# Kernel tuning notes

Measured on AMD Instinct MI355X. Metric: run time of the kernel, lower is better.

## Reference

```python
import jax, jax.numpy as jnp
import numpy as np

N = 8192
IN_DIM = 512
HID = 256


def _gcn_conv(x, adj, W, b, drop):
    # x: [N, d_in] -> [N, d_out]
    h = jnp.matmul(x, W) + b
    if drop:
        return h
    # adj_hat = adj + I; deg = rowsum(adj_hat); out = D^-1/2 adj_hat D^-1/2 h
    deg = jnp.sum(adj, axis=1) + 1.0  # +1 from identity
    dinv = jnp.where(deg > 0, deg ** -0.5, 0.0)  # [N]
    hs = dinv[:, None] * h
    agg = jnp.matmul(adj, hs) + hs  # (adj + I) @ hs without materializing adj+I
    return dinv[:, None] * agg


def _layernorm(x, gamma, beta, eps=1e-6):
    mu = jnp.mean(x, axis=-1, keepdims=True)
    var = jnp.mean((x - mu) ** 2, axis=-1, keepdims=True)
    return (x - mu) * jax.lax.rsqrt(var + eps) * gamma + beta


def setup_inputs() -> dict:
    key = jax.random.key(0)
    ks = jax.random.split(key, 6)
    x = jax.random.normal(ks[0], (N, IN_DIM), dtype=jnp.float32)
    adj = jax.random.uniform(ks[1], (N, N), dtype=jnp.float32)
    W1 = jax.random.normal(ks[2], (IN_DIM, HID), dtype=jnp.float32) * (1.0 / np.sqrt(IN_DIM))
    b1 = jax.random.normal(ks[3], (HID,), dtype=jnp.float32) * 1e-6
    W2 = jax.random.normal(ks[4], (HID, HID), dtype=jnp.float32) * (1.0 / np.sqrt(HID))
    b2 = jax.random.normal(ks[5], (HID,), dtype=jnp.float32) * 1e-6
    ln_gamma = jnp.ones((HID,), dtype=jnp.float32)
    ln_beta = jnp.zeros((HID,), dtype=jnp.float32)
    return {"x": x, "adj": adj, "W1": W1, "b1": b1, "W2": W2, "b2": b2,
            "ln_gamma": ln_gamma, "ln_beta": ln_beta, "drop": 0}


def reference(x, adj, W1, b1, W2, b2, ln_gamma, ln_beta, drop):
    h = _gcn_conv(x, adj, W1, b1, drop)
    h = jax.nn.gelu(h, approximate=False)  # torch F.gelu default = exact erf
    h = _layernorm(h, ln_gamma, ln_beta)
    # dropout -> identity (eval / deterministic baseline)
    out = _gcn_conv(h, adj, W2, b2, drop)
    return out
```

## Files before the change

kernel.cpp:

```cpp
#include <hip/hip_runtime.h>
#include <math.h>

typedef __attribute__((ext_vector_type(4))) float f32x4;
typedef __attribute__((ext_vector_type(8))) short s16x8;
typedef __attribute__((ext_vector_type(2))) int i32x2;
typedef __attribute__((ext_vector_type(4))) int i32x4;

#define BM 32
#define BN 256
#define BK 64
#define LDS_TILE ((BM + BN) * BK)

#define BM2 128
#define BN2 256
#define BK2 128
#define KFULL 8192
#define ZSPLIT 4
#define KQ (KFULL / ZSPLIT)
#define ABYTES (BM2 * BK2)
#define BBYTES (BN2 * BK2)
#define BUFB (ABYTES + BBYTES)

#define SHS 2048.0f
#define INVQ (1.0f / (127.0f * 2048.0f))
#define INVSHS (1.0f / 2048.0f)

__device__ __forceinline__ unsigned short f2bf(float f) {
  unsigned int u = __float_as_uint(f);
  u += 0x7fffu + ((u >> 16) & 1u);
  return (unsigned short)(u >> 16);
}
__device__ __forceinline__ float bf2f(unsigned short h) {
  unsigned int u = ((unsigned int)h) << 16;
  return __uint_as_float(u);
}
__device__ __forceinline__ int rne_i(float x) {
  return __float_as_int(x + 12582912.0f) - 0x4B400000;
}
__device__ __forceinline__ int q_hs(float v) {
  int q = rne_i(v * SHS);
  return q < -127 ? -127 : (q > 127 ? 127 : q);
}
__device__ __forceinline__ void gload16(const void* g, void* l) {
  __builtin_amdgcn_global_load_lds(
      (const __attribute__((address_space(1))) void*)g,
      (__attribute__((address_space(3))) void*)l, 16, 0, 0);
}

__global__ __launch_bounds__(256) void transW(const float* __restrict__ W1,
                                              const float* __restrict__ W2,
                                              float* __restrict__ W1T,
                                              float* __restrict__ W2T) {
  __shared__ float t[64][65];
  int bx = blockIdx.x;
  const float* in;
  float* out;
  int K, M;
  if (bx < 32) { in = W1; out = W1T; K = 512; M = 256; }
  else { bx -= 32; in = W2; out = W2T; K = 256; M = 256; }
  int tiles_m = M >> 6;
  int tk = bx / tiles_m, tm = bx % tiles_m;
  int k0 = tk * 64, m0 = tm * 64;
  int ty = threadIdx.x >> 4, tx = threadIdx.x & 15;
#pragma unroll
  for (int i = 0; i < 4; ++i) {
    f32x4 v = *(const f32x4*)(in + (size_t)(k0 + ty + 16 * i) * M + m0 + tx * 4);
    t[ty + 16 * i][tx * 4 + 0] = v[0];
    t[ty + 16 * i][tx * 4 + 1] = v[1];
    t[ty + 16 * i][tx * 4 + 2] = v[2];
    t[ty + 16 * i][tx * 4 + 3] = v[3];
  }
  __syncthreads();
#pragma unroll
  for (int i = 0; i < 4; ++i) {
    int m = ty + 16 * i;
    f32x4 v = {t[tx * 4 + 0][m], t[tx * 4 + 1][m], t[tx * 4 + 2][m], t[tx * 4 + 3][m]};
    *(f32x4*)(out + (size_t)(m0 + m) * K + k0 + tx * 4) = v;
  }
}

template <bool BF32, int EPI>
__device__ __forceinline__ void gemm_small(int bx, unsigned short* ldsb,
                                           const float* __restrict__ AT,
                                           const void* __restrict__ BTp,
                                           void* __restrict__ outp,
                                           const float* __restrict__ bias,
                                           const float* __restrict__ dinv,
                                           int M, int N, int K) {
  const int tid = threadIdx.x;
  const int m0 = (bx & (M / BM - 1)) * BM;
  const int n0 = (bx / (M / BM)) * BN;
  const int sr = tid >> 3;
  const int sc = (tid & 7) * 8;
  const float* Bf = (const float*)BTp;
  const unsigned short* Bh = (const unsigned short*)BTp;

  f32x4 a_f[2];
  f32x4 b_f[8][2];
  s16x8 b_h[8];

  auto stage_load = [&](int k0) {
    const float* pa = AT + (size_t)(m0 + sr) * K + k0 + sc;
    a_f[0] = *(const f32x4*)(pa);
    a_f[1] = *(const f32x4*)(pa + 4);
#pragma unroll
    for (int it = 0; it < 8; ++it) {
      int n = n0 + it * 32 + sr;
      if (BF32) {
        const float* p = Bf + (size_t)n * K + k0 + sc;
        b_f[it][0] = *(const f32x4*)(p);
        b_f[it][1] = *(const f32x4*)(p + 4);
      } else {
        b_h[it] = *(const s16x8*)(Bh + (size_t)n * K + k0 + sc);
      }
    }
  };

  auto stage_write = [&](int buf) {
    unsigned short* L = ldsb + buf * LDS_TILE;
    {
      s16x8 v;
#pragma unroll
      for (int j = 0; j < 8; ++j) v[j] = (short)f2bf(j < 4 ? a_f[0][j] : a_f[1][j - 4]);
      int idx = (sr * BK + sc) ^ ((sr & 7) << 3);
      *(s16x8*)(L + idx) = v;
    }
#pragma unroll
    for (int it = 0; it < 8; ++it) {
      int r = it * 32 + sr;
      s16x8 w;
      if (BF32) {
#pragma unroll
        for (int j = 0; j < 8; ++j)
          w[j] = (short)f2bf(j < 4 ? b_f[it][0][j] : b_f[it][1][j - 4]);
      } else {
        w = b_h[it];
      }
      int idx = BM * BK + ((r * BK + sc) ^ ((r & 7) << 3));
      *(s16x8*)(L + idx) = w;
    }
  };

  const int lane = tid & 63;
  const int wv = tid >> 6;
  const int g = lane >> 4, lr = lane & 15;

  int aidx[2][2], bidx[4][2];
#pragma unroll
  for (int m = 0; m < 2; ++m)
#pragma unroll
    for (int ks = 0; ks < 2; ++ks) {
      int r = m * 16 + lr;
      aidx[m][ks] = (r * BK + ks * 32 + g * 8) ^ ((r & 7) << 3);
    }
#pragma unroll
  for (int n = 0; n < 4; ++n)
#pragma unroll
    for (int ks = 0; ks < 2; ++ks) {
      int r = wv * 64 + n * 16 + lr;
      bidx[n][ks] = BM * BK + ((r * BK + ks * 32 + g * 8) ^ ((r & 7) << 3));
    }

  f32x4 acc[2][4];
#pragma unroll
  for (int m = 0; m < 2; ++m)
#pragma unroll
    for (int n = 0; n < 4; ++n) {
      f32x4 z = {0.f, 0.f, 0.f, 0.f};
      acc[m][n] = z;
    }

  auto compute = [&](int buf) {
    const unsigned short* L = ldsb + buf * LDS_TILE;
    s16x8 af[2][2], bfr[4][2];
#pragma unroll
    for (int m = 0; m < 2; ++m)
#pragma unroll
      for (int ks = 0; ks < 2; ++ks) af[m][ks] = *(const s16x8*)(L + aidx[m][ks]);
#pragma unroll
    for (int n = 0; n < 4; ++n)
#pragma unroll
      for (int ks = 0; ks < 2; ++ks) bfr[n][ks] = *(const s16x8*)(L + bidx[n][ks]);
#pragma unroll
    for (int m = 0; m < 2; ++m)
#pragma unroll
      for (int n = 0; n < 4; ++n)
#pragma unroll
        for (int ks = 0; ks < 2; ++ks)
          acc[m][n] = __builtin_amdgcn_mfma_f32_16x16x32_bf16(af[m][ks], bfr[n][ks],
                                                              acc[m][n], 0, 0, 0);
  };

  stage_load(0);
  stage_write(0);
  __syncthreads();
  int cur = 0;
  const int nt = K / BK;
  for (int t = 0; t < nt; ++t) {
    if (t + 1 < nt) stage_load((t + 1) * BK);
    compute(cur);
    if (t + 1 < nt) {
      stage_write(cur ^ 1);
      __syncthreads();
      cur ^= 1;
    }
  }

#pragma unroll
  for (int m = 0; m < 2; ++m)
#pragma unroll
    for (int n = 0; n < 4; ++n) {
      int col = n0 + wv * 64 + n * 16 + lr;
#pragma unroll
      for (int r = 0; r < 4; ++r) {
        int row = m0 + m * 16 + g * 4 + r;
        float v = acc[m][n][r];
        if constexpr (EPI == 3) {
          ((unsigned short*)outp)[(size_t)row * N + col] = f2bf(v + bias[row]);
        } else {
          int q = q_hs((v + bias[row]) * dinv[col]);
          ((char*)outp)[(size_t)row * N + col] = (char)q;
        }
      }
    }
}

__global__ __launch_bounds__(256) void prep(const float* __restrict__ adj,
                                            const float* __restrict__ x,
                                            const float* __restrict__ W1T,
                                            const float* __restrict__ b1,
                                            char* __restrict__ adjq,
                                            float* __restrict__ dinv,
                                            unsigned short* __restrict__ h1) {
  __shared__ unsigned short lds[2 * LDS_TILE];
  int bx = blockIdx.x;
  if (bx < 256) {
    gemm_small<true, 3>(bx, lds, W1T, x, h1, b1, nullptr, 256, 8192, 512);
    return;
  }
  bx -= 256;
  float* smf = (float*)lds;
  const int tid = threadIdx.x;
  float psum[2];
#pragma unroll
  for (int rr = 0; rr < 2; ++rr) {
    int row = bx * 2 + rr;
    const float* src = adj + (size_t)row * 8192;
    char* dst = adjq + (size_t)row * 8192;
    float s = 0.f;
    for (int c = tid * 8; c < 8192; c += 2048) {
      f32x4 v0 = __builtin_nontemporal_load((const f32x4*)(src + c));
      f32x4 v1 = __builtin_nontemporal_load((const f32x4*)(src + c + 4));
      s += v0[0] + v0[1] + v0[2] + v0[3] + v1[0] + v1[1] + v1[2] + v1[3];
      i32x2 o;
      o[0] = (rne_i(v0[0] * 127.f) & 0xff) | ((rne_i(v0[1] * 127.f) & 0xff) << 8) |
             ((rne_i(v0[2] * 127.f) & 0xff) << 16) | (rne_i(v0[3] * 127.f) << 24);
      o[1] = (rne_i(v1[0] * 127.f) & 0xff) | ((rne_i(v1[1] * 127.f) & 0xff) << 8) |
             ((rne_i(v1[2] * 127.f) & 0xff) << 16) | (rne_i(v1[3] * 127.f) << 24);
      *(i32x2*)(dst + c) = o;
    }
    psum[rr] = s;
  }
#pragma unroll
  for (int rr = 0; rr < 2; ++rr) {
    float s = psum[rr];
#pragma unroll
    for (int off = 32; off > 0; off >>= 1) s += __shfl_down(s, off, 64);
    if ((tid & 63) == 0) smf[rr * 4 + (tid >> 6)] = s;
  }
  __syncthreads();
  if (tid < 2) {
    float tot = smf[tid * 4] + smf[tid * 4 + 1] + smf[tid * 4 + 2] + smf[tid * 4 + 3];
    dinv[bx * 2 + tid] = rsqrtf(tot + 1.0f);
  }
}

__global__ __launch_bounds__(256) void scale_i8(const unsigned short* __restrict__ h1,
                                                const float* __restrict__ dinv,
                                                char* __restrict__ hq1) {
  size_t e = ((size_t)blockIdx.x * 256 + threadIdx.x) * 16;
  int k = (int)(e & 8191);
  s16x8 v0 = *(const s16x8*)(h1 + e);
  s16x8 v1 = *(const s16x8*)(h1 + e + 8);
  i32x4 o;
#pragma unroll
  for (int q = 0; q < 4; ++q) {
    f32x4 d = *(const f32x4*)(dinv + k + q * 4);
    const s16x8& v = (q < 2) ? v0 : v1;
    int b = (q & 1) * 4;
    int q0 = q_hs(bf2f((unsigned short)v[b + 0]) * d[0]);
    int q1 = q_hs(bf2f((unsigned short)v[b + 1]) * d[1]);
    int q2 = q_hs(bf2f((unsigned short)v[b + 2]) * d[2]);
    int q3 = q_hs(bf2f((unsigned short)v[b + 3]) * d[3]);
    o[q] = (q0 & 0xff) | ((q1 & 0xff) << 8) | ((q2 & 0xff) << 16) | (q3 << 24);
  }
  *(i32x4*)(hq1 + e) = o;
}

__global__ __launch_bounds__(512) void gemm_big(const char* __restrict__ A,
                                                const char* __restrict__ B,
                                                int* __restrict__ P) {
  __shared__ char lds[3 * BUFB];
  const int tid = threadIdx.x;
  const int mt = blockIdx.x & 63;
  const int z = blockIdx.x >> 6;
  const int m0 = mt * BM2;

  const int trow = tid >> 3;
  const int srcgr = (tid & 7) ^ (trow & 7);

  const char* Asrc[2];
#pragma unroll
  for (int j = 0; j < 2; ++j)
    Asrc[j] = A + (size_t)(m0 + j * 64 + trow) * KFULL + (size_t)z * KQ + srcgr * 16;
  const char* Bsrc[4];
#pragma unroll
  for (int j = 0; j < 4; ++j)
    Bsrc[j] = B + (size_t)(j * 64 + trow) * KFULL + (size_t)z * KQ + srcgr * 16;

  auto stage = [&](int buf, int t) {
    char* L = lds + buf * BUFB;
#pragma unroll
    for (int j = 0; j < 2; ++j)
      gload16(Asrc[j] + (size_t)t * BK2, L + (j * 512 + tid) * 16);
#pragma unroll
    for (int j = 0; j < 4; ++j)
      gload16(Bsrc[j] + (size_t)t * BK2, L + ABYTES + (j * 512 + tid) * 16);
  };

  const int w = tid >> 6, l = tid & 63;
  const int wr = w >> 2, wc = w & 3;
  const int g = l >> 4, lr = l & 15;
  int aoff[4][2], boff[4][2];
#pragma unroll
  for (int m = 0; m < 4; ++m)
#pragma unroll
    for (int ks = 0; ks < 2; ++ks) {
      int r = wr * 64 + m * 16 + lr;
      aoff[m][ks] = r * BK2 + (((ks * 4 + g) ^ (r & 7)) * 16);
    }
#pragma unroll
  for (int n = 0; n < 4; ++n)
#pragma unroll
    for (int ks = 0; ks < 2; ++ks) {
      int r = wc * 64 + n * 16 + lr;
      boff[n][ks] = ABYTES + r * BK2 + (((ks * 4 + g) ^ (r & 7)) * 16);
    }

  i32x4 acc[4][4];
#pragma unroll
  for (int m = 0; m < 4; ++m)
#pragma unroll
    for (int n = 0; n < 4; ++n) {
      i32x4 zz = {0, 0, 0, 0};
      acc[m][n] = zz;
    }

  stage(0, 0);
  stage(1, 1);

  const int nt = KQ / BK2;
  for (int t = 0; t < nt; ++t) {
    int cur = t % 3;
    if (t + 1 < nt) asm volatile("s_waitcnt vmcnt(6)" ::: "memory");
    else            asm volatile("s_waitcnt vmcnt(0)" ::: "memory");
    asm volatile("s_barrier" ::: "memory");
    __builtin_amdgcn_sched_barrier(0);

    const char* L = lds + cur * BUFB;
    i32x4 af[4][2], bfr[4][2];
#pragma unroll
    for (int m = 0; m < 4; ++m)
#pragma unroll
      for (int ks = 0; ks < 2; ++ks) af[m][ks] = *(const i32x4*)(L + aoff[m][ks]);
#pragma unroll
    for (int n = 0; n < 4; ++n)
#pragma unroll
      for (int ks = 0; ks < 2; ++ks) bfr[n][ks] = *(const i32x4*)(L + boff[n][ks]);

    if (t + 2 < nt) stage((t + 2) % 3, t + 2);

    __builtin_amdgcn_s_setprio(1);
#pragma unroll
    for (int m = 0; m < 4; ++m)
#pragma unroll
      for (int n = 0; n < 4; ++n)
#pragma unroll
        for (int ks = 0; ks < 2; ++ks)
          acc[m][n] = __builtin_amdgcn_mfma_i32_16x16x64_i8(af[m][ks], bfr[n][ks],
                                                            acc[m][n], 0, 0, 0);
    __builtin_amdgcn_s_setprio(0);
  }

  int* Pz = P + (size_t)z * 8192 * 256;
#pragma unroll
  for (int m = 0; m < 4; ++m)
#pragma unroll
    for (int n = 0; n < 4; ++n) {
      int col = wc * 64 + n * 16 + lr;
#pragma unroll
      for (int r = 0; r < 4; ++r) {
        int row = m0 + wr * 64 + m * 16 + g * 4 + r;
        Pz[(size_t)row * 256 + col] = acc[m][n][r];
      }
    }
}

__global__ __launch_bounds__(256) void reduce_ln(const int* __restrict__ P,
                                                 const unsigned short* __restrict__ h1,
                                                 const float* __restrict__ dinv,
                                                 const float* __restrict__ gamma,
                                                 const float* __restrict__ beta,
                                                 unsigned short* __restrict__ hln) {
  const size_t ZSTR = (size_t)8192 * 256;
  int row = blockIdx.x * 4 + (threadIdx.x >> 6);
  int l = threadIdx.x & 63;
  const int* p = P + (size_t)row * 256 + l * 4;
  i32x4 a = *(const i32x4*)p;
  i32x4 b = *(const i32x4*)(p + ZSTR);
  i32x4 c = *(const i32x4*)(p + 2 * ZSTR);
  i32x4 d = *(const i32x4*)(p + 3 * ZSTR);
  float di = dinv[row];
  float gl[4];
  float s = 0.f, q = 0.f;
#pragma unroll
  for (int j = 0; j < 4; ++j) {
    int h = l * 4 + j;
    float agg = (float)(a[j] + b[j] + c[j] + d[j]) * INVQ;
    float hsv = bf2f(h1[(size_t)h * 8192 + row]) * di;
    float v = (agg + hsv) * di;
    float gv = 0.5f * v * (1.0f + erff(v * 0.70710678118654752440f));
    gl[j] = gv;
    s += gv;
    q += gv * gv;
  }
#pragma unroll
  for (int off = 1; off < 64; off <<= 1) {
    s += __shfl_xor(s, off, 64);
    q += __shfl_xor(q, off, 64);
  }
  float mu = s * (1.0f / 256.0f);
  float var = q * (1.0f / 256.0f) - mu * mu;
  float rs = rsqrtf(fmaxf(var, 0.f) + 1e-6f);
  f32x4 gm = *(const f32x4*)(gamma + l * 4);
  f32x4 bt = *(const f32x4*)(beta + l * 4);
  unsigned short o4[4];
#pragma unroll
  for (int j = 0; j < 4; ++j)
    o4[j] = f2bf((gl[j] - mu) * rs * gm[j] + bt[j]);
  *(unsigned long long*)(hln + (size_t)row * 256 + l * 4) =
      *(const unsigned long long*)o4;
}

__global__ __launch_bounds__(256) void reduce_sc(const int* __restrict__ P,
                                                 const char* __restrict__ hq2,
                                                 const float* __restrict__ dinv,
                                                 float* __restrict__ out) {
  const size_t ZSTR = (size_t)8192 * 256;
  int row = blockIdx.x * 4 + (threadIdx.x >> 6);
  int l = threadIdx.x & 63;
  const int* p = P + (size_t)row * 256 + l * 4;
  i32x4 a = *(const i32x4*)p;
  i32x4 b = *(const i32x4*)(p + ZSTR);
  i32x4 c = *(const i32x4*)(p + 2 * ZSTR);
  i32x4 d = *(const i32x4*)(p + 3 * ZSTR);
  float di = dinv[row];
  f32x4 o;
#pragma unroll
  for (int j = 0; j < 4; ++j) {
    int h = l * 4 + j;
    float agg = (float)(a[j] + b[j] + c[j] + d[j]) * INVQ;
    float hsv = (float)((signed char)hq2[(size_t)h * 8192 + row]) * INVSHS;
    o[j] = (agg + hsv) * di;
  }
  *(f32x4*)(out + (size_t)row * 256 + l * 4) = o;
}

__global__ __launch_bounds__(256) void gemm6_k(const float* __restrict__ W2T,
                                               const unsigned short* __restrict__ hln,
                                               char* __restrict__ hq2,
                                               const float* __restrict__ b2,
                                               const float* __restrict__ dinv) {
  __shared__ unsigned short lds[2 * LDS_TILE];
  gemm_small<false, 6>(blockIdx.x, lds, W2T, hln, hq2, b2, dinv, 256, 8192, 256);
}

extern "C" void kernel_launch(void* const* d_in, const int* in_sizes, int n_in,
                              void* d_out, int out_size, void* d_ws, size_t ws_size,
                              hipStream_t stream) {
  (void)in_sizes; (void)n_in; (void)out_size; (void)ws_size;
  const float* x     = (const float*)d_in[0];
  const float* adj   = (const float*)d_in[1];
  const float* W1    = (const float*)d_in[2];
  const float* b1    = (const float*)d_in[3];
  const float* W2    = (const float*)d_in[4];
  const float* b2    = (const float*)d_in[5];
  const float* gamma = (const float*)d_in[6];
  const float* beta  = (const float*)d_in[7];
  float* out = (float*)d_out;

  char* ws = (char*)d_ws;
  float* dinv          = (float*)ws;
  float* W1T           = (float*)(ws + (64 << 10));
  float* W2T           = (float*)(ws + (640 << 10));
  unsigned short* h1   = (unsigned short*)(ws + (1 << 20));
  char* hq1            = (char*)(ws + (8 << 20));
  unsigned short* hln  = (unsigned short*)(ws + (12 << 20));
  char* hq2            = (char*)(ws + (20 << 20));
  int* P               = (int*)(ws + (32 << 20));
  char* adjq           = (char*)(ws + (64 << 20));

  transW<<<48, 256, 0, stream>>>(W1, W2, W1T, W2T);
  prep<<<4352, 256, 0, stream>>>(adj, x, W1T, b1, adjq, dinv, h1);
  scale_i8<<<512, 256, 0, stream>>>(h1, dinv, hq1);
  gemm_big<<<256, 512, 0, stream>>>(adjq, hq1, P);
  reduce_ln<<<2048, 256, 0, stream>>>(P, h1, dinv, gamma, beta, hln);
  gemm6_k<<<256, 256, 0, stream>>>(W2T, hln, hq2, b2, dinv);
  gemm_big<<<256, 512, 0, stream>>>(adjq, hq2, P);
  reduce_sc<<<2048, 256, 0, stream>>>(P, hq2, dinv, out);
}
```

Measured before the change: 177.7 us.

## Emit int16 split-K partials and node-major quantized features for coalesced reductions

The first big GEMM now writes its split-K partial sums as int16, rounded and shifted by 6 bits and staged through LDS for coalesced stores, which halves the partial-buffer traffic read by reduce_ln. The scaling and second small-GEMM kernels also write a transposed node-major copy of the quantized features. The reduction kernels then read the self-loop term contiguously instead of with strided column gathers. This costs extra LDS staging and transposed writes, and the 16-bit partials lose precision and could clip if sums exceed the int16 range.

```diff
diff --git a/kernel.cpp b/kernel.cpp
--- a/kernel.cpp
+++ b/kernel.cpp
@@ -3,6 +3,7 @@
 
 typedef __attribute__((ext_vector_type(4))) float f32x4;
 typedef __attribute__((ext_vector_type(8))) short s16x8;
+typedef __attribute__((ext_vector_type(4))) short s16x4;
 typedef __attribute__((ext_vector_type(2))) int i32x2;
 typedef __attribute__((ext_vector_type(4))) int i32x4;
 
@@ -22,7 +23,8 @@
 #define BUFB (ABYTES + BBYTES)
 
 #define SHS 2048.0f
-#define INVQ (1.0f / (127.0f * 2048.0f))
+#define SINV16 (64.0f / (127.0f * 2048.0f))
+#define SINV32 (1.0f / (127.0f * 2048.0f))
 #define INVSHS (1.0f / 2048.0f)
 
 __device__ __forceinline__ unsigned short f2bf(float f) {
@@ -84,6 +86,7 @@
                                            const float* __restrict__ AT,
                                            const void* __restrict__ BTp,
                                            void* __restrict__ outp,
+                                           char* __restrict__ outn,
                                            const float* __restrict__ bias,
                                            const float* __restrict__ dinv,
                                            int M, int N, int K) {
@@ -206,23 +209,42 @@
     }
   }
 
-#pragma unroll
-  for (int m = 0; m < 2; ++m)
-#pragma unroll
-    for (int n = 0; n < 4; ++n) {
-      int col = n0 + wv * 64 + n * 16 + lr;
-#pragma unroll
-      for (int r = 0; r < 4; ++r) {
-        int row = m0 + m * 16 + g * 4 + r;
-        float v = acc[m][n][r];
-        if constexpr (EPI == 3) {
-          ((unsigned short*)outp)[(size_t)row * N + col] = f2bf(v + bias[row]);
-        } else {
-          int q = q_hs((v + bias[row]) * dinv[col]);
-          ((char*)outp)[(size_t)row * N + col] = (char)q;
+  if constexpr (EPI == 3) {
+#pragma unroll
+    for (int m = 0; m < 2; ++m)
+#pragma unroll
+      for (int n = 0; n < 4; ++n) {
+        int col = n0 + wv * 64 + n * 16 + lr;
+#pragma unroll
+        for (int r = 0; r < 4; ++r) {
+          int row = m0 + m * 16 + g * 4 + r;
+          ((unsigned short*)outp)[(size_t)row * N + col] = f2bf(acc[m][n][r] + bias[row]);
         }
       }
-    }
+  } else {
+    __syncthreads();
+    char* T2 = (char*)ldsb;
+#pragma unroll
+    for (int m = 0; m < 2; ++m)
+#pragma unroll
+      for (int n = 0; n < 4; ++n) {
+        int cl = wv * 64 + n * 16 + lr;
+        float dv = dinv[n0 + cl];
+#pragma unroll
+        for (int r = 0; r < 4; ++r) {
+          int rl = m * 16 + g * 4 + r;
+          int q = q_hs((acc[m][n][r] + bias[m0 + rl]) * dv);
+          T2[cl * 48 + rl] = (char)q;
+          ((char*)outp)[(size_t)(m0 + rl) * N + n0 + cl] = (char)q;
+        }
+      }
+    __syncthreads();
+#pragma unroll
+    for (int h = 0; h < 2; ++h) {
+      i32x4 vv = *(const i32x4*)(T2 + tid * 48 + h * 16);
+      *(i32x4*)(outn + (size_t)(n0 + tid) * 256 + m0 + h * 16) = vv;
+    }
+  }
 }
 
 __global__ __launch_bounds__(256) void prep(const float* __restrict__ adj,
@@ -235,7 +257,7 @@
   __shared__ unsigned short lds[2 * LDS_TILE];
   int bx = blockIdx.x;
   if (bx < 256) {
-    gemm_small<true, 3>(bx, lds, W1T, x, h1, b1, nullptr, 256, 8192, 512);
+    gemm_small<true, 3>(bx, lds, W1T, x, h1, nullptr, b1, nullptr, 256, 8192, 512);
     return;
   }
   bx -= 256;
@@ -275,31 +297,45 @@
   }
 }
 
-__global__ __launch_bounds__(256) void scale_i8(const unsigned short* __restrict__ h1,
+__global__ __launch_bounds__(256) void scale_tr(const unsigned short* __restrict__ h1,
                                                 const float* __restrict__ dinv,
-                                                char* __restrict__ hq1) {
-  size_t e = ((size_t)blockIdx.x * 256 + threadIdx.x) * 16;
-  int k = (int)(e & 8191);
-  s16x8 v0 = *(const s16x8*)(h1 + e);
-  s16x8 v1 = *(const s16x8*)(h1 + e + 8);
-  i32x4 o;
-#pragma unroll
-  for (int q = 0; q < 4; ++q) {
-    f32x4 d = *(const f32x4*)(dinv + k + q * 4);
-    const s16x8& v = (q < 2) ? v0 : v1;
-    int b = (q & 1) * 4;
-    int q0 = q_hs(bf2f((unsigned short)v[b + 0]) * d[0]);
-    int q1 = q_hs(bf2f((unsigned short)v[b + 1]) * d[1]);
-    int q2 = q_hs(bf2f((unsigned short)v[b + 2]) * d[2]);
-    int q3 = q_hs(bf2f((unsigned short)v[b + 3]) * d[3]);
-    o[q] = (q0 & 0xff) | ((q1 & 0xff) << 8) | ((q2 & 0xff) << 16) | (q3 << 24);
-  }
-  *(i32x4*)(hq1 + e) = o;
-}
-
+                                                char* __restrict__ hq1,
+                                                char* __restrict__ hq1n) {
+  __shared__ char Tq[64][80];
+  int nt_ = blockIdx.x >> 2, ht = blockIdx.x & 3;
+  int n0 = nt_ * 64, h0 = ht * 64;
+  const int tid = threadIdx.x;
+  const int c8 = (tid & 7) * 8;
+  f32x4 d0 = *(const f32x4*)(dinv + n0 + c8);
+  f32x4 d1 = *(const f32x4*)(dinv + n0 + c8 + 4);
+#pragma unroll
+  for (int it = 0; it < 2; ++it) {
+    int hh = (tid >> 3) + it * 32;
+    s16x8 v = *(const s16x8*)(h1 + (size_t)(h0 + hh) * 8192 + n0 + c8);
+    unsigned int lo = 0, hi = 0;
+#pragma unroll
+    for (int j = 0; j < 8; ++j) {
+      float dv = (j < 4) ? d0[j] : d1[j - 4];
+      int q = q_hs(bf2f((unsigned short)v[j]) * dv);
+      Tq[c8 + j][hh] = (char)q;
+      if (j < 4) lo |= ((unsigned int)(q & 0xff)) << (8 * j);
+      else       hi |= ((unsigned int)(q & 0xff)) << (8 * (j - 4));
+    }
+    i32x2 o;
+    o[0] = (int)lo;
+    o[1] = (int)hi;
+    *(i32x2*)(hq1 + (size_t)(h0 + hh) * 8192 + n0 + c8) = o;
+  }
+  __syncthreads();
+  int node = tid >> 2, h16 = (tid & 3) * 16;
+  i32x4 vv = *(const i32x4*)(&Tq[node][h16]);
+  *(i32x4*)(hq1n + (size_t)(n0 + node) * 256 + h0 + h16) = vv;
+}
+
+template <bool P16OUT>
 __global__ __launch_bounds__(512) void gemm_big(const char* __restrict__ A,
                                                 const char* __restrict__ B,
-                                                int* __restrict__ P) {
+                                                void* __restrict__ Pout) {
   __shared__ char lds[3 * BUFB];
   const int tid = threadIdx.x;
   const int mt = blockIdx.x & 63;
@@ -392,22 +428,49 @@
     __builtin_amdgcn_s_setprio(0);
   }
 
-  int* Pz = P + (size_t)z * 8192 * 256;
-#pragma unroll
-  for (int m = 0; m < 4; ++m)
-#pragma unroll
-    for (int n = 0; n < 4; ++n) {
-      int col = wc * 64 + n * 16 + lr;
-#pragma unroll
-      for (int r = 0; r < 4; ++r) {
-        int row = m0 + wr * 64 + m * 16 + g * 4 + r;
-        Pz[(size_t)row * 256 + col] = acc[m][n][r];
+  if constexpr (!P16OUT) {
+    int* Pz = (int*)Pout + (size_t)z * 8192 * 256;
+#pragma unroll
+    for (int m = 0; m < 4; ++m)
+#pragma unroll
+      for (int n = 0; n < 4; ++n) {
+        int col = wc * 64 + n * 16 + lr;
+#pragma unroll
+        for (int r = 0; r < 4; ++r) {
+          int row = m0 + wr * 64 + m * 16 + g * 4 + r;
+          Pz[(size_t)row * 256 + col] = acc[m][n][r];
+        }
       }
-    }
-}
-
-__global__ __launch_bounds__(256) void reduce_ln(const int* __restrict__ P,
-                                                 const unsigned short* __restrict__ h1,
+  } else {
+    __syncthreads();
+    unsigned short* Tp = (unsigned short*)lds;
+#pragma unroll
+    for (int m = 0; m < 4; ++m)
+#pragma unroll
+      for (int n = 0; n < 4; ++n) {
+        int cl = wc * 64 + n * 16 + lr;
+#pragma unroll
+        for (int r = 0; r < 4; ++r) {
+          int rl = wr * 64 + m * 16 + g * 4 + r;
+          int v = (acc[m][n][r] + 32) >> 6;
+          v = v < -32768 ? -32768 : (v > 32767 ? 32767 : v);
+          Tp[rl * 264 + cl] = (unsigned short)(short)v;
+        }
+      }
+    __syncthreads();
+    short* Pz = (short*)Pout + (size_t)z * 8192 * 256 + (size_t)m0 * 256;
+#pragma unroll
+    for (int pass = 0; pass < 8; ++pass) {
+      int c = pass * 512 + tid;
+      int r = c >> 5, off = (c & 31) * 8;
+      s16x8 v = *(const s16x8*)(Tp + r * 264 + off);
+      *(s16x8*)(Pz + (size_t)c * 8) = v;
+    }
+  }
+}
+
+__global__ __launch_bounds__(256) void reduce_ln(const short* __restrict__ P16,
+                                                 const char* __restrict__ hq1n,
                                                  const float* __restrict__ dinv,
                                                  const float* __restrict__ gamma,
                                                  const float* __restrict__ beta,
@@ -415,19 +478,19 @@
   const size_t ZSTR = (size_t)8192 * 256;
   int row = blockIdx.x * 4 + (threadIdx.x >> 6);
   int l = threadIdx.x & 63;
-  const int* p = P + (size_t)row * 256 + l * 4;
-  i32x4 a = *(const i32x4*)p;
-  i32x4 b = *(const i32x4*)(p + ZSTR);
-  i32x4 c = *(const i32x4*)(p + 2 * ZSTR);
-  i32x4 d = *(const i32x4*)(p + 3 * ZSTR);
+  const short* p = P16 + (size_t)row * 256 + l * 4;
+  s16x4 a = *(const s16x4*)p;
+  s16x4 b = *(const s16x4*)(p + ZSTR);
+  s16x4 c = *(const s16x4*)(p + 2 * ZSTR);
+  s16x4 d = *(const s16x4*)(p + 3 * ZSTR);
+  int q4 = *(const int*)(hq1n + (size_t)row * 256 + l * 4);
   float di = dinv[row];
   float gl[4];
   float s = 0.f, q = 0.f;
 #pragma unroll
   for (int j = 0; j < 4; ++j) {
-    int h = l * 4 + j;
-    float agg = (float)(a[j] + b[j] + c[j] + d[j]) * INVQ;
-    float hsv = bf2f(h1[(size_t)h * 8192 + row]) * di;
+    float agg = (float)((int)a[j] + b[j] + c[j] + d[j]) * SINV16;
+    float hsv = (float)((signed char)(q4 >> (8 * j))) * INVSHS;
     float v = (agg + hsv) * di;
     float gv = 0.5f * v * (1.0f + erff(v * 0.70710678118654752440f));
     gl[j] = gv;
@@ -452,25 +515,25 @@
       *(const unsigned long long*)o4;
 }
 
-__global__ __launch_bounds__(256) void reduce_sc(const int* __restrict__ P,
-                                                 const char* __restrict__ hq2,
+__global__ __launch_bounds__(256) void reduce_sc(const int* __restrict__ P32,
+                                                 const char* __restrict__ hq2n,
                                                  const float* __restrict__ dinv,
                                                  float* __restrict__ out) {
   const size_t ZSTR = (size_t)8192 * 256;
   int row = blockIdx.x * 4 + (threadIdx.x >> 6);
   int l = threadIdx.x & 63;
-  const int* p = P + (size_t)row * 256 + l * 4;
+  const int* p = P32 + (size_t)row * 256 + l * 4;
   i32x4 a = *(const i32x4*)p;
   i32x4 b = *(const i32x4*)(p + ZSTR);
   i32x4 c = *(const i32x4*)(p + 2 * ZSTR);
   i32x4 d = *(const i32x4*)(p + 3 * ZSTR);
+  int q4 = *(const int*)(hq2n + (size_t)row * 256 + l * 4);
   float di = dinv[row];
   f32x4 o;
 #pragma unroll
   for (int j = 0; j < 4; ++j) {
-    int h = l * 4 + j;
-    float agg = (float)(a[j] + b[j] + c[j] + d[j]) * INVQ;
-    float hsv = (float)((signed char)hq2[(size_t)h * 8192 + row]) * INVSHS;
+    float agg = (float)(a[j] + b[j] + c[j] + d[j]) * SINV32;
+    float hsv = (float)((signed char)(q4 >> (8 * j))) * INVSHS;
     o[j] = (agg + hsv) * di;
   }
   *(f32x4*)(out + (size_t)row * 256 + l * 4) = o;
@@ -479,10 +542,11 @@
 __global__ __launch_bounds__(256) void gemm6_k(const float* __restrict__ W2T,
                                                const unsigned short* __restrict__ hln,
                                                char* __restrict__ hq2,
+                                               char* __restrict__ hq2n,
                                                const float* __restrict__ b2,
                                                const float* __restrict__ dinv) {
   __shared__ unsigned short lds[2 * LDS_TILE];
-  gemm_small<false, 6>(blockIdx.x, lds, W2T, hln, hq2, b2, dinv, 256, 8192, 256);
+  gemm_small<false, 6>(blockIdx.x, lds, W2T, hln, hq2, hq2n, b2, dinv, 256, 8192, 256);
 }
 
 extern "C" void kernel_launch(void* const* d_in, const int* in_sizes, int n_in,
@@ -505,17 +569,19 @@
   float* W2T           = (float*)(ws + (640 << 10));
   unsigned short* h1   = (unsigned short*)(ws + (1 << 20));
   char* hq1            = (char*)(ws + (8 << 20));
-  unsigned short* hln  = (unsigned short*)(ws + (12 << 20));
+  char* hq1n           = (char*)(ws + (10 << 20));
+  unsigned short* hln  = (unsigned short*)(ws + (14 << 20));
   char* hq2            = (char*)(ws + (20 << 20));
-  int* P               = (int*)(ws + (32 << 20));
+  char* hq2n           = (char*)(ws + (24 << 20));
+  void* P              = (void*)(ws + (32 << 20));
   char* adjq           = (char*)(ws + (64 << 20));
 
   transW<<<48, 256, 0, stream>>>(W1, W2, W1T, W2T);
   prep<<<4352, 256, 0, stream>>>(adj, x, W1T, b1, adjq, dinv, h1);
-  scale_i8<<<512, 256, 0, stream>>>(h1, dinv, hq1);
-  gemm_big<<<256, 512, 0, stream>>>(adjq, hq1, P);
-  reduce_ln<<<2048, 256, 0, stream>>>(P, h1, dinv, gamma, beta, hln);
-  gemm6_k<<<256, 256, 0, stream>>>(W2T, hln, hq2, b2, dinv);
-  gemm_big<<<256, 512, 0, stream>>>(adjq, hq2, P);
-  reduce_sc<<<2048, 256, 0, stream>>>(P, hq2, dinv, out);
-}
+  scale_tr<<<512, 256, 0, stream>>>(h1, dinv, hq1, hq1n);
+  gemm_big<true><<<256, 512, 0, stream>>>(adjq, hq1, P);
+  reduce_ln<<<2048, 256, 0, stream>>>((const short*)P, hq1n, dinv, gamma, beta, hln);
+  gemm6_k<<<256, 256, 0, stream>>>(W2T, hln, hq2, hq2n, b2, dinv);
+  gemm_big<false><<<256, 512, 0, stream>>>(adjq, hq2, P);
+  reduce_sc<<<2048, 256, 0, stream>>>((const int*)P, hq2n, dinv, out);
+}
```

Result: faster. 161.4 us (-9.1%).
